# Performance work log

Hardware: AMD Instinct MI355X
Metric: run time of the kernel (lower is better)

## Reference

```python
import jax, jax.numpy as jnp
import numpy as np

N_NODES = 50000
N_EDGES = 800000
N_FEAT = 128
HIDDEN = 64
N_CLASSES = 16


def setup_inputs() -> dict:
    key = jax.random.key(0)
    ks = jax.random.split(key, 8)
    x = jax.random.normal(ks[0], (N_NODES, N_FEAT), dtype=jnp.float32)
    edge_index = jax.random.randint(ks[1], (2, N_EDGES), 0, N_NODES, dtype=jnp.int64)
    # GCNConv weights (glorot-like) and biases
    W1 = jax.random.normal(ks[2], (N_FEAT, HIDDEN), dtype=jnp.float32) / np.sqrt(N_FEAT)
    b1 = jnp.zeros((HIDDEN,), dtype=jnp.float32)
    W2 = jax.random.normal(ks[3], (HIDDEN, HIDDEN), dtype=jnp.float32) / np.sqrt(HIDDEN)
    b2 = jnp.zeros((HIDDEN,), dtype=jnp.float32)
    Wout = jax.random.normal(ks[4], (HIDDEN, N_CLASSES), dtype=jnp.float32) / np.sqrt(HIDDEN)
    bout = jnp.zeros((N_CLASSES,), dtype=jnp.float32)
    return {"x": x, "edge_index": edge_index, "W1": W1, "b1": b1,
            "W2": W2, "b2": b2, "Wout": Wout, "bout": bout}


def _gcn_conv(h, src, dst, norm, W, b, n_nodes):
    # h: [N, F_in]; linear transform then normalized scatter-add aggregation
    h = h @ W                                   # [N, F_out]
    msg = h[src] * norm[:, None]                # gather + scale  [E+N, F_out]
    out = jax.ops.segment_sum(msg, dst, num_segments=n_nodes)  # scatter-add
    return out + b


def reference(x, edge_index, W1, b1, W2, b2, Wout, bout):
    n = x.shape[0]
    # add self-loops (PyG GCNConv default add_self_loops=True)
    loops = jnp.arange(n, dtype=edge_index.dtype)
    src = jnp.concatenate([edge_index[0], loops])
    dst = jnp.concatenate([edge_index[1], loops])
    # symmetric normalization: deg^-1/2[src] * deg^-1/2[dst] (edge_weight = 1)
    ones = jnp.ones(src.shape[0], dtype=x.dtype)
    deg = jax.ops.segment_sum(ones, dst, num_segments=n)
    dinv = jnp.where(deg > 0, jax.lax.rsqrt(jnp.maximum(deg, 1e-12)), 0.0)
    norm = dinv[src] * dinv[dst]

    h = _gcn_conv(x, src, dst, norm, W1, b1, n)
    h = jax.nn.relu(h)
    # dropout p=0.5 with training=False -> identity
    h = _gcn_conv(h, src, dst, norm, W2, b2, n)
    h = jax.nn.relu(h)
    logits = h @ Wout + bout
    return jax.nn.softmax(logits, axis=1)
```

## Files before the change

### kernel.cpp

```cpp
#include <hip/hip_runtime.h>
#include <hip/hip_fp16.h>

#define N_NODES 50000
#define N_EDGES 800000
#define N_FEAT 128
#define HIDDEN 64
#define N_CLASSES 16
#define NBLK_NODE 196
#define TCAP 8192

typedef _Float16 f16x8 __attribute__((ext_vector_type(8)));
typedef float f32x4 __attribute__((ext_vector_type(4)));

__global__ void k_init(int* __restrict__ tileCur) {
    int tid = threadIdx.x;
    if (tid < NBLK_NODE) tileCur[tid] = tid * TCAP;
}

__global__ __launch_bounds__(256) void k_part(const int* __restrict__ ei,
                                              int* __restrict__ tileCur,
                                              int* __restrict__ binned) {
    __shared__ int cnt[NBLK_NODE], base[NBLK_NODE], cur[NBLK_NODE];
    int tid = threadIdx.x;
    int start = blockIdx.x * 4096;
    if (tid < NBLK_NODE) cnt[tid] = 0;
    __syncthreads();
    int s[16], d[16];
#pragma unroll
    for (int u = 0; u < 4; ++u) {
        int e0 = start + u * 1024 + tid * 4;
        if (e0 + 4 <= N_EDGES) {
            int4 s4 = *(const int4*)&ei[e0];
            int4 d4 = *(const int4*)&ei[N_EDGES + e0];
            s[u * 4 + 0] = s4.x; s[u * 4 + 1] = s4.y; s[u * 4 + 2] = s4.z; s[u * 4 + 3] = s4.w;
            d[u * 4 + 0] = d4.x; d[u * 4 + 1] = d4.y; d[u * 4 + 2] = d4.z; d[u * 4 + 3] = d4.w;
#pragma unroll
            for (int q = 0; q < 4; ++q) atomicAdd(&cnt[d[u * 4 + q] >> 8], 1);
        } else {
#pragma unroll
            for (int q = 0; q < 4; ++q) {
                int e = e0 + q;
                if (e < N_EDGES) {
                    s[u * 4 + q] = ei[e];
                    d[u * 4 + q] = ei[N_EDGES + e];
                    atomicAdd(&cnt[d[u * 4 + q] >> 8], 1);
                } else s[u * 4 + q] = -1;
            }
        }
    }
    __syncthreads();
    if (tid < NBLK_NODE) {
        base[tid] = atomicAdd(&tileCur[tid], cnt[tid]);
        cur[tid] = 0;
    }
    __syncthreads();
#pragma unroll
    for (int u = 0; u < 16; ++u) {
        if (s[u] < 0) continue;
        int t = d[u] >> 8;
        int r = atomicAdd(&cur[t], 1);
        int p = base[t] + r;
        if (p < (t + 1) * TCAP)
            binned[p] = s[u] | ((d[u] & 255) << 16);
    }
}

__device__ __forceinline__ void finesort_body(int tb, const int* __restrict__ binned,
                                              const int* __restrict__ tileCur,
                                              int* __restrict__ csr,
                                              int2* __restrict__ rse,
                                              float* __restrict__ dinv, char* smem) {
    int* stage   = (int*)smem;
    int* sc      = stage + TCAP;
    int* cnt256  = sc + 256;
    int* nodeOff = cnt256 + 256;
    int tid = threadIdx.x;
    int beg = tb * TCAP;
    int m = tileCur[tb] - beg;
    if (m > TCAP) m = TCAP;
    cnt256[tid] = 0;
    __syncthreads();
    const int4* b4 = (const int4*)(binned + beg);
    int nv = m >> 2;
    for (int i = tid; i < nv; i += 256) {
        int4 r = b4[i];
        atomicAdd(&cnt256[(r.x >> 16) & 255], 1);
        atomicAdd(&cnt256[(r.y >> 16) & 255], 1);
        atomicAdd(&cnt256[(r.z >> 16) & 255], 1);
        atomicAdd(&cnt256[(r.w >> 16) & 255], 1);
    }
    for (int i = (m & ~3) + tid; i < m; i += 256)
        atomicAdd(&cnt256[(binned[beg + i] >> 16) & 255], 1);
    __syncthreads();
    int myc = cnt256[tid];
    sc[tid] = myc;
    __syncthreads();
#pragma unroll
    for (int off = 1; off < 256; off <<= 1) {
        int t = (tid >= off) ? sc[tid - off] : 0;
        __syncthreads();
        sc[tid] += t;
        __syncthreads();
    }
    int off0 = sc[tid] - myc;
    nodeOff[tid] = off0;
    int gnode = tb * 256 + tid;
    if (gnode < N_NODES) {
        dinv[gnode] = rsqrtf((float)myc + 1.0f);
        rse[gnode] = make_int2(beg + off0, myc);
    }
    cnt256[tid] = 0;
    __syncthreads();
    for (int i = tid; i < nv; i += 256) {
        int4 r = b4[i];
        int rr;
        rr = atomicAdd(&cnt256[(r.x >> 16) & 255], 1); stage[nodeOff[(r.x >> 16) & 255] + rr] = r.x & 0xFFFF;
        rr = atomicAdd(&cnt256[(r.y >> 16) & 255], 1); stage[nodeOff[(r.y >> 16) & 255] + rr] = r.y & 0xFFFF;
        rr = atomicAdd(&cnt256[(r.z >> 16) & 255], 1); stage[nodeOff[(r.z >> 16) & 255] + rr] = r.z & 0xFFFF;
        rr = atomicAdd(&cnt256[(r.w >> 16) & 255], 1); stage[nodeOff[(r.w >> 16) & 255] + rr] = r.w & 0xFFFF;
    }
    for (int i = (m & ~3) + tid; i < m; i += 256) {
        int rec = binned[beg + i];
        int dl = (rec >> 16) & 255;
        int rr = atomicAdd(&cnt256[dl], 1);
        stage[nodeOff[dl] + rr] = rec & 0xFFFF;
    }
    __syncthreads();
    int4* c4 = (int4*)(csr + beg);
    for (int i = tid; i < nv; i += 256) c4[i] = ((const int4*)stage)[i];
    for (int i = (m & ~3) + tid; i < m; i += 256) csr[beg + i] = stage[i];
}

template <int K, typename TIn>
__device__ __forceinline__ void mm_body(int bx, const TIn* __restrict__ a,
                                        const float* __restrict__ w,
                                        __half* __restrict__ out, char* smem) {
    constexpr int LDK = K + 8;
    __half* A_lds  = (__half*)smem;
    __half* Wt_lds = A_lds + 64 * LDK;
    int tid = threadIdx.x;
    long nbase = (long)bx * 64;

    for (int i = tid; i < K * 16; i += 256) {
        int k = (i * 4) >> 6;
        int f0 = (i * 4) & 63;
        float4 v = *(const float4*)&w[i * 4];
        Wt_lds[(f0 + 0) * LDK + k] = __float2half(v.x);
        Wt_lds[(f0 + 1) * LDK + k] = __float2half(v.y);
        Wt_lds[(f0 + 2) * LDK + k] = __float2half(v.z);
        Wt_lds[(f0 + 3) * LDK + k] = __float2half(v.w);
    }
    for (int i = tid; i < 64 * K / 8; i += 256) {
        int n = (i * 8) / K;
        int k0 = (i * 8) % K;
        long gn = nbase + n;
        if constexpr (sizeof(TIn) == 4) {
            float4 v0, v1;
            if (gn < N_NODES) {
                v0 = *(const float4*)&a[gn * K + k0];
                v1 = *(const float4*)&a[gn * K + k0 + 4];
            } else {
                v0 = make_float4(0.f, 0.f, 0.f, 0.f);
                v1 = v0;
            }
            __half2* dst = (__half2*)&A_lds[n * LDK + k0];
            dst[0] = __floats2half2_rn(v0.x, v0.y);
            dst[1] = __floats2half2_rn(v0.z, v0.w);
            dst[2] = __floats2half2_rn(v1.x, v1.y);
            dst[3] = __floats2half2_rn(v1.z, v1.w);
        } else {
            int4 v = (gn < N_NODES) ? *(const int4*)&a[gn * K + k0]
                                    : make_int4(0, 0, 0, 0);
            *(int4*)&A_lds[n * LDK + k0] = v;
        }
    }
    __syncthreads();

    int wv = tid >> 6;
    int lane = tid & 63;
    int m = lane & 15;
    int quad = lane >> 4;
    const __half* Arow = &A_lds[(wv * 16 + m) * LDK + quad * 8];
    f32x4 acc[4] = {};
#pragma unroll
    for (int t = 0; t < K; t += 32) {
        f16x8 af = *(const f16x8*)(const void*)&Arow[t];
#pragma unroll
        for (int g = 0; g < 4; ++g) {
            f16x8 bf = *(const f16x8*)(const void*)&Wt_lds[(g * 16 + m) * LDK + t + quad * 8];
            acc[g] = __builtin_amdgcn_mfma_f32_16x16x32_f16(af, bf, acc[g], 0, 0, 0);
        }
    }

#pragma unroll
    for (int r = 0; r < 4; ++r) {
        int n = wv * 16 + quad * 4 + r;
        long gn = nbase + n;
        if (gn < N_NODES) {
#pragma unroll
            for (int g = 0; g < 4; ++g)
                out[gn * HIDDEN + g * 16 + m] = __float2half(acc[g][r]);
        }
    }
}

__global__ __launch_bounds__(256) void k_fsmm1(const int* __restrict__ binned,
                                               const int* __restrict__ tileCur,
                                               int* __restrict__ csr,
                                               int2* __restrict__ rse,
                                               float* __restrict__ dinv,
                                               const float* __restrict__ x,
                                               const float* __restrict__ W1,
                                               __half* __restrict__ bufA) {
    __shared__ __align__(16) char smem[35840];
    int bx = blockIdx.x;
    if (bx < NBLK_NODE)
        finesort_body(bx, binned, tileCur, csr, rse, dinv, smem);
    else
        mm_body<N_FEAT, float>(bx - NBLK_NODE, x, W1, bufA, smem);
}

__global__ __launch_bounds__(256) void k_mm2(const __half* __restrict__ a,
                                             const float* __restrict__ w,
                                             __half* __restrict__ out) {
    __shared__ __align__(16) char smem[2 * 64 * (HIDDEN + 8) * 2];
    mm_body<HIDDEN, __half>(blockIdx.x, a, w, out, smem);
}

__device__ __forceinline__ void acc_row8s(float* a, int4 rv, float s) {
    float2 f;
    f = __half22float2(*(__half2*)&rv.x); a[0] = fmaf(f.x, s, a[0]); a[1] = fmaf(f.y, s, a[1]);
    f = __half22float2(*(__half2*)&rv.y); a[2] = fmaf(f.x, s, a[2]); a[3] = fmaf(f.y, s, a[3]);
    f = __half22float2(*(__half2*)&rv.z); a[4] = fmaf(f.x, s, a[4]); a[5] = fmaf(f.y, s, a[5]);
    f = __half22float2(*(__half2*)&rv.w); a[6] = fmaf(f.x, s, a[6]); a[7] = fmaf(f.y, s, a[7]);
}

__global__ void k_gather(const __half* __restrict__ h, const int* __restrict__ csr,
                         const int2* __restrict__ rse, const float* __restrict__ dinv,
                         const float* __restrict__ bias, __half* __restrict__ out) {
    int t = blockIdx.x * 256 + threadIdx.x;
    int node = __builtin_amdgcn_readfirstlane(t >> 6);
    int lane = t & 63;
    int e8 = lane >> 3;
    int q = lane & 7;
    int2 se = rse[node];
    int r0 = se.x, r1 = se.x + se.y;
    float dd = dinv[node];

    float a[8] = {0.f, 0.f, 0.f, 0.f, 0.f, 0.f, 0.f, 0.f};
    if (e8 == 0)
        acc_row8s(a, *(const int4*)&h[(long)node * HIDDEN + q * 8], dd);

    int j = r0;
    while (j + 16 <= r1) {
        int sA = csr[j + e8];
        int sB = csr[j + 8 + e8];
        float dA = dinv[sA];
        float dB = dinv[sB];
        int4 rA = *(const int4*)&h[(long)sA * HIDDEN + q * 8];
        int4 rB = *(const int4*)&h[(long)sB * HIDDEN + q * 8];
        acc_row8s(a, rA, dA);
        acc_row8s(a, rB, dB);
        j += 16;
    }
    if (j + 8 <= r1) {
        int sA = csr[j + e8];
        float dA = dinv[sA];
        acc_row8s(a, *(const int4*)&h[(long)sA * HIDDEN + q * 8], dA);
        j += 8;
    }
    int rem = r1 - j;
    if (e8 < rem) {
        int sA = csr[j + e8];
        float dA = dinv[sA];
        acc_row8s(a, *(const int4*)&h[(long)sA * HIDDEN + q * 8], dA);
    }
#pragma unroll
    for (int off = 8; off < 64; off <<= 1)
#pragma unroll
        for (int i = 0; i < 8; ++i) a[i] += __shfl_xor(a[i], off, 64);

    if (e8 == 0) {
        float4 b0 = *(const float4*)&bias[q * 8];
        float4 b1 = *(const float4*)&bias[q * 8 + 4];
        float r[8];
        r[0] = fmaxf(fmaf(a[0], dd, b0.x), 0.f);
        r[1] = fmaxf(fmaf(a[1], dd, b0.y), 0.f);
        r[2] = fmaxf(fmaf(a[2], dd, b0.z), 0.f);
        r[3] = fmaxf(fmaf(a[3], dd, b0.w), 0.f);
        r[4] = fmaxf(fmaf(a[4], dd, b1.x), 0.f);
        r[5] = fmaxf(fmaf(a[5], dd, b1.y), 0.f);
        r[6] = fmaxf(fmaf(a[6], dd, b1.z), 0.f);
        r[7] = fmaxf(fmaf(a[7], dd, b1.w), 0.f);
        __half2 h0 = __floats2half2_rn(r[0], r[1]);
        __half2 h1 = __floats2half2_rn(r[2], r[3]);
        __half2 h2 = __floats2half2_rn(r[4], r[5]);
        __half2 h3 = __floats2half2_rn(r[6], r[7]);
        int4 o;
        o.x = *(int*)&h0; o.y = *(int*)&h1; o.z = *(int*)&h2; o.w = *(int*)&h3;
        *(int4*)&out[(long)node * HIDDEN + q * 8] = o;
    }
}

__global__ void k_out(const __half* __restrict__ h, const float* __restrict__ w,
                      const float* __restrict__ b, float* __restrict__ out) {
    __shared__ float Ws[HIDDEN * N_CLASSES];
    __shared__ float bs[N_CLASSES];
    int tid = threadIdx.x;
    for (int i = tid; i < HIDDEN * N_CLASSES; i += 256) Ws[i] = w[i];
    if (tid < N_CLASSES) bs[tid] = b[tid];
    __syncthreads();
    int node = blockIdx.x * 16 + (tid >> 4);
    int c = tid & 15;
    const __half* hr = h + (long)node * HIDDEN;
    float acc = bs[c];
#pragma unroll
    for (int k = 0; k < HIDDEN; ++k)
        acc = fmaf(__half2float(hr[k]), Ws[k * N_CLASSES + c], acc);
    float m = acc;
#pragma unroll
    for (int off = 8; off; off >>= 1) m = fmaxf(m, __shfl_xor(m, off, 16));
    float ex = expf(acc - m);
    float s = ex;
#pragma unroll
    for (int off = 8; off; off >>= 1) s += __shfl_xor(s, off, 16);
    out[(long)node * N_CLASSES + c] = ex / s;
}

extern "C" void kernel_launch(void* const* d_in, const int* in_sizes, int n_in,
                              void* d_out, int out_size, void* d_ws, size_t ws_size,
                              hipStream_t stream) {
    const float* x    = (const float*)d_in[0];
    const int*   ei   = (const int*)d_in[1];
    const float* W1   = (const float*)d_in[2];
    const float* b1   = (const float*)d_in[3];
    const float* W2   = (const float*)d_in[4];
    const float* b2   = (const float*)d_in[5];
    const float* Wout = (const float*)d_in[6];
    const float* bout = (const float*)d_in[7];
    float* out = (float*)d_out;

    char* ws = (char*)d_ws;
    int2*   rse     = (int2*)ws;                       ws += 400128;
    float*  dinv    = (float*)ws;                      ws += 200192;
    int*    tileCur = (int*)ws;                        ws += 1024;
    int*    csr     = (int*)ws;                        ws += (size_t)NBLK_NODE * TCAP * 4;
    int*    binned  = (int*)ws;                        ws += (size_t)NBLK_NODE * TCAP * 4;
    __half* bufA    = (__half*)ws;                     ws += 6553600;
    __half* bufB    = (__half*)ws;

    const int NB_MM = (N_NODES + 63) / 64;
    const int NB_E16 = (N_EDGES + 4095) / 4096;

    k_init<<<1, 256, 0, stream>>>(tileCur);
    k_part<<<NB_E16, 256, 0, stream>>>(ei, tileCur, binned);

    k_fsmm1<<<NBLK_NODE + NB_MM, 256, 0, stream>>>(binned, tileCur, csr, rse, dinv,
                                                   x, W1, bufA);

    k_gather<<<N_NODES / 4, 256, 0, stream>>>(bufA, csr, rse, dinv, b1, bufB);

    k_mm2<<<NB_MM, 256, 0, stream>>>(bufB, W2, bufA);
    k_gather<<<N_NODES / 4, 256, 0, stream>>>(bufA, csr, rse, dinv, b2, bufB);

    k_out<<<N_NODES / 16, 256, 0, stream>>>(bufB, Wout, bout, out);
}
```

Measured before the change: 164.7 us.

## Prescale layer-2 features by dinv and issue edge gathers up front

The second GEMM now multiplies each output row by dinv of its source node, so the second gather no longer has to load dinv[src] per edge and can accumulate plain sums. The gather kernel is also restructured to issue the first 32 neighbor index and row loads up front with predicates, replacing the dependent 16-edge loop, which exposes more memory-level parallelism for typical degrees (about 17 on average). The cost is extra registers and predicated loads for low-degree nodes, and a change in where fp16 rounding happens.

Result: no change. 164.7 us (-0.0%).

```diff
diff --git a/kernel.cpp b/kernel.cpp
--- a/kernel.cpp
+++ b/kernel.cpp
@@ -134,6 +134,7 @@
 template <int K, typename TIn>
 __device__ __forceinline__ void mm_body(int bx, const TIn* __restrict__ a,
                                         const float* __restrict__ w,
+                                        const float* __restrict__ dscale,
                                         __half* __restrict__ out, char* smem) {
     constexpr int LDK = K + 8;
     __half* A_lds  = (__half*)smem;
@@ -197,9 +198,10 @@
         int n = wv * 16 + quad * 4 + r;
         long gn = nbase + n;
         if (gn < N_NODES) {
+            float di = dscale ? dscale[gn] : 1.0f;
 #pragma unroll
             for (int g = 0; g < 4; ++g)
-                out[gn * HIDDEN + g * 16 + m] = __float2half(acc[g][r]);
+                out[gn * HIDDEN + g * 16 + m] = __float2half(acc[g][r] * di);
         }
     }
 }
@@ -217,14 +219,15 @@
     if (bx < NBLK_NODE)
         finesort_body(bx, binned, tileCur, csr, rse, dinv, smem);
     else
-        mm_body<N_FEAT, float>(bx - NBLK_NODE, x, W1, bufA, smem);
+        mm_body<N_FEAT, float>(bx - NBLK_NODE, x, W1, nullptr, bufA, smem);
 }
 
 __global__ __launch_bounds__(256) void k_mm2(const __half* __restrict__ a,
                                              const float* __restrict__ w,
+                                             const float* __restrict__ dinv,
                                              __half* __restrict__ out) {
     __shared__ __align__(16) char smem[2 * 64 * (HIDDEN + 8) * 2];
-    mm_body<HIDDEN, __half>(blockIdx.x, a, w, out, smem);
+    mm_body<HIDDEN, __half>(blockIdx.x, a, w, dinv, out, smem);
 }
 
 __device__ __forceinline__ void acc_row8s(float* a, int4 rv, float s) {
@@ -234,7 +237,15 @@
     f = __half22float2(*(__half2*)&rv.z); a[4] = fmaf(f.x, s, a[4]); a[5] = fmaf(f.y, s, a[5]);
     f = __half22float2(*(__half2*)&rv.w); a[6] = fmaf(f.x, s, a[6]); a[7] = fmaf(f.y, s, a[7]);
 }
-
+__device__ __forceinline__ void acc_row8(float* a, int4 rv) {
+    float2 f;
+    f = __half22float2(*(__half2*)&rv.x); a[0] += f.x; a[1] += f.y;
+    f = __half22float2(*(__half2*)&rv.y); a[2] += f.x; a[3] += f.y;
+    f = __half22float2(*(__half2*)&rv.z); a[4] += f.x; a[5] += f.y;
+    f = __half22float2(*(__half2*)&rv.w); a[6] += f.x; a[7] += f.y;
+}
+
+template <bool SCALE>
 __global__ void k_gather(const __half* __restrict__ h, const int* __restrict__ csr,
                          const int2* __restrict__ rse, const float* __restrict__ dinv,
                          const float* __restrict__ bias, __half* __restrict__ out) {
@@ -243,38 +254,51 @@
     int lane = t & 63;
     int e8 = lane >> 3;
     int q = lane & 7;
+
+    int4 vs = make_int4(0, 0, 0, 0);
+    if (e8 == 0) vs = *(const int4*)&h[(long)node * HIDDEN + q * 8];
+    float dd = dinv[node];
     int2 se = rse[node];
-    int r0 = se.x, r1 = se.x + se.y;
-    float dd = dinv[node];
+    int r0 = se.x, deg = se.y;
+
+    bool p0 = e8 < deg, p1 = e8 + 8 < deg, p2 = e8 + 16 < deg, p3 = e8 + 24 < deg;
+    int c0 = 0, c1 = 0, c2 = 0, c3 = 0;
+    if (p0) c0 = csr[r0 + e8];
+    if (p1) c1 = csr[r0 + 8 + e8];
+    if (p2) c2 = csr[r0 + 16 + e8];
+    if (p3) c3 = csr[r0 + 24 + e8];
+
+    int4 v0 = make_int4(0,0,0,0), v1 = v0, v2 = v0, v3 = v0;
+    float d0 = 0.f, d1 = 0.f, d2 = 0.f, d3 = 0.f;
+    if (p0) { v0 = *(const int4*)&h[(long)c0 * HIDDEN + q * 8]; if (SCALE) d0 = dinv[c0]; }
+    if (p1) { v1 = *(const int4*)&h[(long)c1 * HIDDEN + q * 8]; if (SCALE) d1 = dinv[c1]; }
+    if (p2) { v2 = *(const int4*)&h[(long)c2 * HIDDEN + q * 8]; if (SCALE) d2 = dinv[c2]; }
+    if (p3) { v3 = *(const int4*)&h[(long)c3 * HIDDEN + q * 8]; if (SCALE) d3 = dinv[c3]; }
 
     float a[8] = {0.f, 0.f, 0.f, 0.f, 0.f, 0.f, 0.f, 0.f};
-    if (e8 == 0)
-        acc_row8s(a, *(const int4*)&h[(long)node * HIDDEN + q * 8], dd);
-
-    int j = r0;
-    while (j + 16 <= r1) {
-        int sA = csr[j + e8];
-        int sB = csr[j + 8 + e8];
-        float dA = dinv[sA];
-        float dB = dinv[sB];
-        int4 rA = *(const int4*)&h[(long)sA * HIDDEN + q * 8];
-        int4 rB = *(const int4*)&h[(long)sB * HIDDEN + q * 8];
-        acc_row8s(a, rA, dA);
-        acc_row8s(a, rB, dB);
-        j += 16;
-    }
-    if (j + 8 <= r1) {
-        int sA = csr[j + e8];
-        float dA = dinv[sA];
-        acc_row8s(a, *(const int4*)&h[(long)sA * HIDDEN + q * 8], dA);
-        j += 8;
-    }
-    int rem = r1 - j;
-    if (e8 < rem) {
-        int sA = csr[j + e8];
-        float dA = dinv[sA];
-        acc_row8s(a, *(const int4*)&h[(long)sA * HIDDEN + q * 8], dA);
-    }
+    if constexpr (SCALE) {
+        acc_row8s(a, vs, dd);
+        acc_row8s(a, v0, d0);
+        acc_row8s(a, v1, d1);
+        acc_row8s(a, v2, d2);
+        acc_row8s(a, v3, d3);
+    } else {
+        acc_row8(a, vs);
+        acc_row8(a, v0);
+        acc_row8(a, v1);
+        acc_row8(a, v2);
+        acc_row8(a, v3);
+    }
+
+    for (int j = 32; j < deg; j += 8) {
+        if (j + e8 < deg) {
+            int s = csr[r0 + j + e8];
+            int4 rv = *(const int4*)&h[(long)s * HIDDEN + q * 8];
+            if constexpr (SCALE) acc_row8s(a, rv, dinv[s]);
+            else                 acc_row8(a, rv);
+        }
+    }
+
 #pragma unroll
     for (int off = 8; off < 64; off <<= 1)
 #pragma unroll
@@ -358,10 +382,10 @@
     k_fsmm1<<<NBLK_NODE + NB_MM, 256, 0, stream>>>(binned, tileCur, csr, rse, dinv,
                                                    x, W1, bufA);
 
-    k_gather<<<N_NODES / 4, 256, 0, stream>>>(bufA, csr, rse, dinv, b1, bufB);
-
-    k_mm2<<<NB_MM, 256, 0, stream>>>(bufB, W2, bufA);
-    k_gather<<<N_NODES / 4, 256, 0, stream>>>(bufA, csr, rse, dinv, b2, bufB);
+    k_gather<true><<<N_NODES / 4, 256, 0, stream>>>(bufA, csr, rse, dinv, b1, bufB);
+
+    k_mm2<<<NB_MM, 256, 0, stream>>>(bufB, W2, dinv, bufA);
+    k_gather<false><<<N_NODES / 4, 256, 0, stream>>>(bufA, csr, rse, dinv, b2, bufB);
 
     k_out<<<N_NODES / 16, 256, 0, stream>>>(bufB, Wout, bout, out);
 }
```
